# Performance work log

Hardware: AMD Instinct MI355X
Metric: run time of the kernel (lower is better)

The kernel has to match this reference:

```python
import jax, jax.numpy as jnp
import numpy as np

N, IN_SZ, OUT_SZ = 8192, 512, 64

def setup_inputs() -> dict:
    key = jax.random.key(0)
    ks = jax.random.split(key, 7)
    s_in = 1.0 / np.sqrt(IN_SZ)
    inp = {
        "input": jax.random.normal(ks[0], (N, IN_SZ), dtype=jnp.float32),
        "Wq": jax.random.uniform(ks[1], (OUT_SZ, IN_SZ), jnp.float32, -s_in, s_in),
        "bq": jax.random.uniform(ks[2], (OUT_SZ,), jnp.float32, -s_in, s_in),
        "Wk": jax.random.uniform(ks[3], (OUT_SZ, IN_SZ), jnp.float32, -s_in, s_in),
        "bk": jax.random.uniform(ks[4], (OUT_SZ,), jnp.float32, -s_in, s_in),
        "Wv": jax.random.uniform(ks[5], (OUT_SZ, IN_SZ), jnp.float32, -s_in, s_in),
        "bv": jax.random.uniform(ks[6], (OUT_SZ,), jnp.float32, -s_in, s_in),
    }
    return inp

def reference(input, Wq, bq, Wk, bk, Wv, bv):
    # torch nn.Linear: x @ W.T + b
    q = input @ Wq.T + bq  # [N, out]
    k = input @ Wk.T + bk  # [N, out]
    v = input @ Wv.T + bv  # [N, out]
    # NOTE: original module has NO 1/sqrt(d) scaling.
    scores = jax.nn.softmax(q @ k.T, axis=-1)  # [N, N]
    return scores @ v  # [N, out]
```

## Files before the change

kernel.cpp:

```cpp
#include <hip/hip_runtime.h>
#include <math.h>

#define SA_N   8192
#define SA_IN  512
#define SA_D   64
#define G_SPL  16
#define LOG2E  1.44269504f

typedef short s16x8 __attribute__((ext_vector_type(8)));
typedef float f32x16 __attribute__((ext_vector_type(16)));

#define MFMA32(A, B, C) __builtin_amdgcn_mfma_f32_32x32x16_bf16((A), (B), (C), 0, 0, 0)

static __device__ __forceinline__ unsigned short f2bf_rn(float x) {
    unsigned int u = __float_as_uint(x);
    unsigned int r = (u + 0x7FFFu + ((u >> 16) & 1u)) >> 16;
    return (unsigned short)r;
}

static __device__ __forceinline__ void trunc_split(float f, unsigned short* hi, unsigned short* lo) {
    unsigned int u = __float_as_uint(f);
    *hi = (unsigned short)(u >> 16);
    float lf = f - __uint_as_float(u & 0xFFFF0000u);
    *lo = (unsigned short)(__float_as_uint(lf) >> 16);
}

static __device__ __forceinline__ unsigned int pack_hi16(unsigned int u0, unsigned int u1) {
    return __builtin_amdgcn_perm(u1, u0, 0x07060302u);
}

static __device__ __forceinline__ void split8(const float4 a, const float4 b, s16x8* xh, s16x8* xl) {
    union { unsigned int u[4]; s16x8 v; } H, L;
    const float f[8] = {a.x, a.y, a.z, a.w, b.x, b.y, b.z, b.w};
#pragma unroll
    for (int p = 0; p < 4; ++p) {
        const unsigned int u0 = __float_as_uint(f[2 * p]);
        const unsigned int u1 = __float_as_uint(f[2 * p + 1]);
        H.u[p] = pack_hi16(u0, u1);
        const float l0 = f[2 * p]     - __uint_as_float(u0 & 0xFFFF0000u);
        const float l1 = f[2 * p + 1] - __uint_as_float(u1 & 0xFFFF0000u);
        L.u[p] = pack_hi16(__float_as_uint(l0), __float_as_uint(l1));
    }
    *xh = H.v; *xl = L.v;
}

static __device__ __forceinline__ s16x8 pack_rn8(const float4 a, const float4 b) {
    union { unsigned int u[4]; s16x8 v; } P;
    const float f[8] = {a.x, a.y, a.z, a.w, b.x, b.y, b.z, b.w};
#pragma unroll
    for (int p = 0; p < 4; ++p)
        P.u[p] = (unsigned int)f2bf_rn(f[2 * p]) | ((unsigned int)f2bf_rn(f[2 * p + 1]) << 16);
    return P.v;
}

__global__ __launch_bounds__(256, 2) void qkv_kernel(
    const float* __restrict__ in,
    const float* __restrict__ Wq, const float* __restrict__ bq,
    const float* __restrict__ Wk, const float* __restrict__ bk,
    const float* __restrict__ Wv, const float* __restrict__ bv,
    unsigned short* __restrict__ Qhi, unsigned short* __restrict__ Qlo,
    unsigned short* __restrict__ KhiF, unsigned short* __restrict__ VF)
{
    __shared__ float cbuf[2][4][64][20];
    __shared__ __align__(16) unsigned short stage[4096];
    const int t    = threadIdx.x;
    const int w    = t >> 6;
    const int lane = t & 63;
    const int h    = lane >> 5;
    const int q32  = lane & 31;
    const int mat  = blockIdx.x >> 8;
    const int jt   = blockIdx.x & 255;
    const int rows0 = jt * 32;

    const float* W = (mat == 0) ? Wq : (mat == 1 ? Wk : Wv);
    const float* B = (mat == 0) ? bq : (mat == 1 ? bk : bv);

    f32x16 accA[2] = {};
    f32x16 accB[2] = {};

#pragma unroll 2
    for (int ksl = 0; ksl < 8; ++ksl) {
        const int ks = (w << 3) + ksl;
        const float* xp = in + (size_t)(rows0 + q32) * SA_IN + ks * 16 + h * 8;
        const float4 xa = *(const float4*)xp;
        const float4 xb = *(const float4*)(xp + 4);
        s16x8 xh, xl;
        split8(xa, xb, &xh, &xl);
#pragma unroll
        for (int mt = 0; mt < 2; ++mt) {
            const float* wp = W + (size_t)(mt * 32 + q32) * SA_IN + ks * 16 + h * 8;
            const float4 wa = *(const float4*)wp;
            const float4 wb = *(const float4*)(wp + 4);
            if (mat < 2) {
                s16x8 ah, al;
                split8(wa, wb, &ah, &al);
                accA[mt] = MFMA32(ah, xh, accA[mt]);
                accB[mt] = MFMA32(ah, xl, accB[mt]);
                accA[mt] = MFMA32(al, xh, accA[mt]);
            } else {
                const s16x8 ah = pack_rn8(wa, wb);
                accA[mt] = MFMA32(ah, xh, accA[mt]);
            }
        }
    }

#pragma unroll
    for (int mt = 0; mt < 2; ++mt) {
        f32x16 tot = accA[mt];
        if (mat < 2) {
#pragma unroll
            for (int r = 0; r < 16; ++r) tot[r] += accB[mt][r];
        }
#pragma unroll
        for (int rg = 0; rg < 4; ++rg) {
            float4 vv = { tot[4 * rg + 0], tot[4 * rg + 1],
                          tot[4 * rg + 2], tot[4 * rg + 3] };
            *(float4*)&cbuf[mt][w][lane][4 * rg] = vv;
        }
    }
    __syncthreads();
    if (w < 2) {
        const int mt = w;
        float c[16];
#pragma unroll
        for (int rg = 0; rg < 4; ++rg) {
            const float4 s0 = *(const float4*)&cbuf[mt][0][lane][4 * rg];
            const float4 s1 = *(const float4*)&cbuf[mt][1][lane][4 * rg];
            const float4 s2 = *(const float4*)&cbuf[mt][2][lane][4 * rg];
            const float4 s3 = *(const float4*)&cbuf[mt][3][lane][4 * rg];
            c[4 * rg + 0] = (s0.x + s1.x) + (s2.x + s3.x);
            c[4 * rg + 1] = (s0.y + s1.y) + (s2.y + s3.y);
            c[4 * rg + 2] = (s0.z + s1.z) + (s2.z + s3.z);
            c[4 * rg + 3] = (s0.w + s1.w) + (s2.w + s3.w);
        }
#pragma unroll
        for (int r = 0; r < 16; ++r) {
            const int o = mt * 32 + (r & 3) + 8 * (r >> 2) + 4 * h;
            float val = c[r] + B[o];
            if (mat == 0) {
                val *= LOG2E;
                unsigned short hi, lo;
                trunc_split(val, &hi, &lo);
                stage[q32 * 64 + o]        = hi;
                stage[2048 + q32 * 64 + o] = lo;
            } else if (mat == 1) {
                const int kl_ = ((o >> 4) * 64 + ((o >> 3) & 1) * 32 + q32) * 8 + (o & 7);
                stage[kl_] = f2bf_rn(val);
            } else {
                const int hp = (q32 >> 2) & 1;
                const int ip = (q32 & 3) + ((q32 >> 3) & 1) * 4;
                const int vl_ = ((o >> 5) * 2 + (q32 >> 4)) * 512
                              + hp * 256 + (o & 31) * 8 + ip;
                stage[vl_] = f2bf_rn(val);
            }
        }
    }
    __syncthreads();

    {
        const uint4* st4 = (const uint4*)stage;
        if (mat == 0) {
            for (int i = t; i < 512; i += 256) {
                unsigned short* dst = ((i < 256) ? Qhi : Qlo) + (size_t)rows0 * 64 + (i & 255) * 8;
                *(uint4*)dst = st4[i];
            }
        } else if (mat == 1) {
            if (t < 256) *(uint4*)(KhiF + (size_t)jt * 2048 + t * 8) = st4[t];
        } else {
            *(uint4*)(VF + (size_t)jt * 2048 + t * 8) = st4[t];
        }
    }
}

__global__ __launch_bounds__(256, 2) void attn_kernel(
    const unsigned short* __restrict__ Qhi, const unsigned short* __restrict__ Qlo,
    const unsigned short* __restrict__ KhiF, const unsigned short* __restrict__ VF,
    unsigned short* __restrict__ Opart, float* __restrict__ Lpart)
{
    __shared__ __align__(16) unsigned short kbuf[2][2][2048];
    const int t    = threadIdx.x;
    const int w    = t >> 6;
    const int lane = t & 63;
    const int h    = lane >> 5;
    const int q32  = lane & 31;
    const int qb   = blockIdx.x >> 4;
    const int g    = blockIdx.x & 15;
    const int q0   = (qb * 4 + w) * 32;
    const int jt0  = g * 16;

    s16x8 qh[4], ql[4];
#pragma unroll
    for (int s = 0; s < 4; ++s) {
        const size_t off = (size_t)(q0 + q32) * 64 + s * 16 + h * 8;
        qh[s] = *reinterpret_cast<const s16x8*>(Qhi + off);
        ql[s] = *reinterpret_cast<const s16x8*>(Qlo + off);
    }

    {
        const size_t base = (size_t)jt0 * 2048 + t * 8;
        const uint4 a = *(const uint4*)(KhiF + base);
        const uint4 c = *(const uint4*)(VF  + base);
        *(uint4*)&kbuf[0][0][t * 8] = a;
        *(uint4*)&kbuf[0][1][t * 8] = c;
    }
    __syncthreads();

    f32x16 O0 = {}, O1 = {};
    float lsum = 0.f;

    for (int it = 0; it < 16; ++it) {
        const int p = it & 1;

        uint4 na, nc;
        if (it < 15) {
            const size_t base = (size_t)(jt0 + it + 1) * 2048 + t * 8;
            na = *(const uint4*)(KhiF + base);
            nc = *(const uint4*)(VF  + base);
        }

        s16x8 kh[4], vv[4];
#pragma unroll
        for (int s = 0; s < 4; ++s) {
            kh[s] = *(const s16x8*)&kbuf[p][0][(s * 64 + lane) * 8];
            vv[s] = *(const s16x8*)&kbuf[p][1][(s * 64 + lane) * 8];
        }

        f32x16 Sa = {}, Sb = {};
#pragma unroll
        for (int s = 0; s < 4; ++s) {
            Sa = MFMA32(kh[s], qh[s], Sa);
            Sb = MFMA32(kh[s], ql[s], Sb);
        }

        float e[16];
#pragma unroll
        for (int r = 0; r < 16; ++r) e[r] = __builtin_amdgcn_exp2f(Sa[r] + Sb[r]);
        lsum += (((e[0] + e[1]) + (e[2] + e[3])) + ((e[4] + e[5]) + (e[6] + e[7])))
              + (((e[8] + e[9]) + (e[10] + e[11])) + ((e[12] + e[13]) + (e[14] + e[15])));

        union { unsigned int u[4]; s16x8 v; } P0, P1;
#pragma unroll
        for (int j2 = 0; j2 < 4; ++j2) {
            P0.u[j2] = pack_hi16(__float_as_uint(e[2 * j2]),     __float_as_uint(e[2 * j2 + 1]));
            P1.u[j2] = pack_hi16(__float_as_uint(e[8 + 2 * j2]), __float_as_uint(e[8 + 2 * j2 + 1]));
        }

        O0 = MFMA32(vv[0], P0.v, O0);
        O0 = MFMA32(vv[1], P1.v, O0);
        O1 = MFMA32(vv[2], P0.v, O1);
        O1 = MFMA32(vv[3], P1.v, O1);

        if (it < 15) {
            *(uint4*)&kbuf[1 - p][0][t * 8] = na;
            *(uint4*)&kbuf[1 - p][1][t * 8] = nc;
        }
        __syncthreads();
    }

    lsum += __shfl_xor(lsum, 32, 64);

    const size_t qg = (size_t)g * SA_N + q0 + q32;
#pragma unroll
    for (int rg = 0; rg < 4; ++rg) {
        const int d0 = 8 * rg + 4 * h;
        uint2 s0, s1;
        s0.x = (unsigned int)f2bf_rn(O0[4 * rg + 0]) | ((unsigned int)f2bf_rn(O0[4 * rg + 1]) << 16);
        s0.y = (unsigned int)f2bf_rn(O0[4 * rg + 2]) | ((unsigned int)f2bf_rn(O0[4 * rg + 3]) << 16);
        s1.x = (unsigned int)f2bf_rn(O1[4 * rg + 0]) | ((unsigned int)f2bf_rn(O1[4 * rg + 1]) << 16);
        s1.y = (unsigned int)f2bf_rn(O1[4 * rg + 2]) | ((unsigned int)f2bf_rn(O1[4 * rg + 3]) << 16);
        *(uint2*)(Opart + qg * 64 + d0)      = s0;
        *(uint2*)(Opart + qg * 64 + d0 + 32) = s1;
    }
    if (h == 0) Lpart[qg] = lsum;
}

__global__ __launch_bounds__(256) void combine_kernel(
    const unsigned short* __restrict__ Opart, const float* __restrict__ Lpart,
    float* __restrict__ out)
{
    const int tid = blockIdx.x * 256 + threadIdx.x;
    const int q  = tid >> 5;
    const int dp = tid & 31;
    const unsigned int* OP = (const unsigned int*)Opart;
    float s0 = 0.f, s1 = 0.f, lt = 0.f;
#pragma unroll
    for (int g = 0; g < G_SPL; ++g) {
        const unsigned int v = OP[((size_t)g * SA_N + q) * 32 + dp];
        s0 += __uint_as_float(v << 16);
        s1 += __uint_as_float(v & 0xFFFF0000u);
        lt += Lpart[(size_t)g * SA_N + q];
    }
    float2 r = { s0 / lt, s1 / lt };
    *(float2*)&out[(size_t)q * 64 + dp * 2] = r;
}

extern "C" void kernel_launch(void* const* d_in, const int* in_sizes, int n_in,
                              void* d_out, int out_size, void* d_ws, size_t ws_size,
                              hipStream_t stream) {
    const float* input = (const float*)d_in[0];
    const float* Wq    = (const float*)d_in[1];
    const float* bq    = (const float*)d_in[2];
    const float* Wk    = (const float*)d_in[3];
    const float* bk    = (const float*)d_in[4];
    const float* Wv    = (const float*)d_in[5];
    const float* bv    = (const float*)d_in[6];
    float* out = (float*)d_out;

    const size_t SEG = (size_t)SA_N * 64;
    unsigned short* Qhi  = (unsigned short*)d_ws;
    unsigned short* Qlo  = Qhi  + SEG;
    unsigned short* KhiF = Qlo  + SEG;
    unsigned short* VF   = KhiF + SEG;
    unsigned short* Opart = VF  + SEG;
    float*          Lpart = (float*)(Opart + (size_t)G_SPL * SA_N * 64);

    qkv_kernel<<<768, 256, 0, stream>>>(input, Wq, bq, Wk, bk, Wv, bv,
                                        Qhi, Qlo, KhiF, VF);
    attn_kernel<<<64 * G_SPL, 256, 0, stream>>>(Qhi, Qlo, KhiF, VF, Opart, Lpart);
    combine_kernel<<<1024, 256, 0, stream>>>(Opart, Lpart, out);
}
```

Baseline: 127.3 us.

## Load K/V fragments directly from global, drop LDS staging and barriers

Removes the shared-memory double buffer for K and V tiles. Each wave now reads its MFMA fragments straight from global memory (L2/L1 cached), which eliminates the per-iteration __syncthreads. Occupancy in launch bounds rises from 2 to 4 blocks per CU, and s_setprio is wrapped around the MFMA groups. The trade is that each wave in a block re-reads the same K/V tile from global instead of sharing it, and there is no explicit prefetch, so load latency has to be hidden by the extra occupancy.

```diff
diff --git a/kernel.cpp b/kernel.cpp
--- a/kernel.cpp
+++ b/kernel.cpp
@@ -172,12 +172,11 @@
     }
 }
 
-__global__ __launch_bounds__(256, 2) void attn_kernel(
+__global__ __launch_bounds__(256, 4) void attn_kernel(
     const unsigned short* __restrict__ Qhi, const unsigned short* __restrict__ Qlo,
     const unsigned short* __restrict__ KhiF, const unsigned short* __restrict__ VF,
     unsigned short* __restrict__ Opart, float* __restrict__ Lpart)
 {
-    __shared__ __align__(16) unsigned short kbuf[2][2][2048];
     const int t    = threadIdx.x;
     const int w    = t >> 6;
     const int lane = t & 63;
@@ -196,41 +195,29 @@
         ql[s] = *reinterpret_cast<const s16x8*>(Qlo + off);
     }
 
-    {
-        const size_t base = (size_t)jt0 * 2048 + t * 8;
-        const uint4 a = *(const uint4*)(KhiF + base);
-        const uint4 c = *(const uint4*)(VF  + base);
-        *(uint4*)&kbuf[0][0][t * 8] = a;
-        *(uint4*)&kbuf[0][1][t * 8] = c;
-    }
-    __syncthreads();
+    const unsigned short* kp = KhiF + (size_t)jt0 * 2048 + lane * 8;
+    const unsigned short* vp = VF   + (size_t)jt0 * 2048 + lane * 8;
 
     f32x16 O0 = {}, O1 = {};
     float lsum = 0.f;
 
     for (int it = 0; it < 16; ++it) {
-        const int p = it & 1;
-
-        uint4 na, nc;
-        if (it < 15) {
-            const size_t base = (size_t)(jt0 + it + 1) * 2048 + t * 8;
-            na = *(const uint4*)(KhiF + base);
-            nc = *(const uint4*)(VF  + base);
-        }
-
         s16x8 kh[4], vv[4];
 #pragma unroll
         for (int s = 0; s < 4; ++s) {
-            kh[s] = *(const s16x8*)&kbuf[p][0][(s * 64 + lane) * 8];
-            vv[s] = *(const s16x8*)&kbuf[p][1][(s * 64 + lane) * 8];
-        }
+            kh[s] = *(const s16x8*)(kp + s * 512);
+            vv[s] = *(const s16x8*)(vp + s * 512);
+        }
+        kp += 2048; vp += 2048;
 
         f32x16 Sa = {}, Sb = {};
+        __builtin_amdgcn_s_setprio(1);
 #pragma unroll
         for (int s = 0; s < 4; ++s) {
             Sa = MFMA32(kh[s], qh[s], Sa);
             Sb = MFMA32(kh[s], ql[s], Sb);
         }
+        __builtin_amdgcn_s_setprio(0);
 
         float e[16];
 #pragma unroll
@@ -245,16 +232,12 @@
             P1.u[j2] = pack_hi16(__float_as_uint(e[8 + 2 * j2]), __float_as_uint(e[8 + 2 * j2 + 1]));
         }
 
+        __builtin_amdgcn_s_setprio(1);
         O0 = MFMA32(vv[0], P0.v, O0);
         O0 = MFMA32(vv[1], P1.v, O0);
         O1 = MFMA32(vv[2], P0.v, O1);
         O1 = MFMA32(vv[3], P1.v, O1);
-
-        if (it < 15) {
-            *(uint4*)&kbuf[1 - p][0][t * 8] = na;
-            *(uint4*)&kbuf[1 - p][1][t * 8] = nc;
-        }
-        __syncthreads();
+        __builtin_amdgcn_s_setprio(0);
     }
 
     lsum += __shfl_xor(lsum, 32, 64);
```

Result: slower. 133.3 us (+4.7%).
